# Optimization experiments

Measured on AMD Instinct MI355X. Metric: run time of the kernel, lower is better.

The kernel has to match this reference:

```python
import jax, jax.numpy as jnp
import numpy as np

N_NODES = 50000
N_EDGES = 25000
N_PAIRS = 800000
D = 96


def setup_inputs() -> dict:
    key = jax.random.key(0)
    ks = jax.random.split(key, 7)
    X = jax.random.normal(ks[0], (N_NODES, D), dtype=jnp.float32)
    X0 = jax.random.normal(ks[1], (N_NODES, D), dtype=jnp.float32)
    W = jax.random.normal(ks[2], (D, D), dtype=jnp.float32) / np.sqrt(D)
    degE = jax.random.uniform(ks[3], (N_EDGES, 1), dtype=jnp.float32, minval=0.1, maxval=1.0)
    degV = jax.random.uniform(ks[4], (N_NODES, 1), dtype=jnp.float32, minval=0.1, maxval=1.0)
    vertex = jax.random.randint(ks[5], (N_PAIRS,), 0, N_NODES, dtype=jnp.int32)
    edges = jax.random.randint(ks[6], (N_PAIRS,), 0, N_EDGES, dtype=jnp.int32)
    return {"X": X, "X0": X0, "W": W, "degE": degE, "degV": degV,
            "vertex": vertex, "edges": edges, "alpha": 0.1, "beta": 0.5}


def reference(X, X0, W, degE, degV, vertex, edges, alpha, beta):
    N = X.shape[0]
    E = degE.shape[0]
    # V -> E hop: gather node features per incidence pair, mean-reduce per hyperedge
    Xve = X[vertex]                                                  # [M, D]
    esum = jax.ops.segment_sum(Xve, edges, num_segments=E)           # [E, D]
    cnt = jax.ops.segment_sum(jnp.ones((edges.shape[0], 1), X.dtype), edges, num_segments=E)
    Xe = esum / jnp.maximum(cnt, 1.0)                                # mean aggregate
    Xe = Xe * degE
    # E -> V hop: gather hyperedge features, sum-reduce per node
    Xev = Xe[edges]                                                  # [M, D]
    Xv = jax.ops.segment_sum(Xev, vertex, num_segments=N)            # [N, D]
    Xv = Xv * degV
    # row L2 normalize (norm is detached in the original)
    rownorm = jnp.linalg.norm(Xv, axis=1, keepdims=True)
    scale = jax.lax.stop_gradient(jnp.where(rownorm > 0, 1.0 / rownorm, 0.0))
    Xn = Xv * scale
    # GCNII-style residual + identity-mapped Linear (bias=False)
    Xi = (1.0 - alpha) * Xn + alpha * X0
    return (1.0 - beta) * Xi + beta * (Xi @ W.T)
```

## Files before the change

kernel.cpp:

```cpp
#include <hip/hip_runtime.h>

#define DD 96
#define DQ 24
#define DC 12
#define SE 80
#define SV 48

typedef __attribute__((ext_vector_type(8))) unsigned short u16x8;
typedef __attribute__((ext_vector_type(8))) short s16x8;
typedef __attribute__((ext_vector_type(4))) float f32x4;

__device__ __forceinline__ unsigned short f2bf(float f) {
    unsigned int u = __builtin_bit_cast(unsigned int, f);
    u += 0x7FFFu + ((u >> 16) & 1u);
    return (unsigned short)(u >> 16);
}
__device__ __forceinline__ float bf2f(unsigned short h) {
    unsigned int u = ((unsigned int)h) << 16;
    return __builtin_bit_cast(float, u);
}

__global__ void hist_conv_k(const int* __restrict__ vtx, const int* __restrict__ edg,
                            int* __restrict__ cntV, int* __restrict__ cntE,
                            unsigned int* __restrict__ rank, int M,
                            const float4* __restrict__ X, u16x8* __restrict__ Xb, int n8,
                            const float* __restrict__ W, const float* __restrict__ beta_p,
                            unsigned short* __restrict__ Mm) {
    int t = blockIdx.x * 256 + threadIdx.x;
    bool doConv = (t < n8);
    float4 a, b;
    if (doConv) {
        a = X[(size_t)t * 2];
        b = X[(size_t)t * 2 + 1];
    }
    bool doHist = (t < M);
    unsigned rE = 0, rV = 0;
    if (doHist) {
        int e = edg[t];
        int v = vtx[t];
        rE = atomicAdd(&cntE[e << 2], 1);
        rV = atomicAdd(&cntV[v << 2], 1);
    }
    if (doConv) {
        u16x8 o;
        o[0] = f2bf(a.x); o[1] = f2bf(a.y); o[2] = f2bf(a.z); o[3] = f2bf(a.w);
        o[4] = f2bf(b.x); o[5] = f2bf(b.y); o[6] = f2bf(b.z); o[7] = f2bf(b.w);
        Xb[t] = o;
    } else if (t < n8 + DD * DD) {
        int i = t - n8;
        int c = i / DD;
        int k = i - c * DD;
        float m = beta_p[0] * W[i];
        if (c == k) m += 1.0f - beta_p[0];
        Mm[i] = f2bf(m);
    }
    if (doHist) rank[t] = (rE & 0xFFFFu) | (rV << 16);
}

__global__ void build_k(const int* __restrict__ vtx, const int* __restrict__ edg,
                        const unsigned int* __restrict__ rank,
                        unsigned short* __restrict__ vlist,
                        unsigned short* __restrict__ elist, int M) {
    int t = blockIdx.x * blockDim.x + threadIdx.x;
    int m0 = t * 4;
    if (m0 + 3 < M) {
        int4 v4 = *(const int4*)(vtx + m0);
        int4 e4 = *(const int4*)(edg + m0);
        uint4 r4 = *(const uint4*)(rank + m0);
        unsigned rE0 = r4.x & 0xFFFFu, rV0 = r4.x >> 16;
        unsigned rE1 = r4.y & 0xFFFFu, rV1 = r4.y >> 16;
        unsigned rE2 = r4.z & 0xFFFFu, rV2 = r4.z >> 16;
        unsigned rE3 = r4.w & 0xFFFFu, rV3 = r4.w >> 16;
        if (rE0 < SE) vlist[e4.x * SE + rE0] = (unsigned short)v4.x;
        if (rE1 < SE) vlist[e4.y * SE + rE1] = (unsigned short)v4.y;
        if (rE2 < SE) vlist[e4.z * SE + rE2] = (unsigned short)v4.z;
        if (rE3 < SE) vlist[e4.w * SE + rE3] = (unsigned short)v4.w;
        if (rV0 < SV) elist[v4.x * SV + rV0] = (unsigned short)e4.x;
        if (rV1 < SV) elist[v4.y * SV + rV1] = (unsigned short)e4.y;
        if (rV2 < SV) elist[v4.z * SV + rV2] = (unsigned short)e4.z;
        if (rV3 < SV) elist[v4.w * SV + rV3] = (unsigned short)e4.w;
    } else {
        for (int m = m0; m < M; ++m) {
            int v = vtx[m], e = edg[m];
            unsigned r = rank[m];
            unsigned rE = r & 0xFFFFu, rV = r >> 16;
            if (rE < SE) vlist[e * SE + rE] = (unsigned short)v;
            if (rV < SV) elist[v * SV + rV] = (unsigned short)e;
        }
    }
}

__global__ __launch_bounds__(256) void gather_ve_w(const u16x8* __restrict__ Xb,
                                                   const int* __restrict__ cntE,
                                                   const unsigned short* __restrict__ vlist,
                                                   const float* __restrict__ degE,
                                                   u16x8* __restrict__ Xe, int E) {
    int wid = threadIdx.x >> 6;
    int lane = threadIdx.x & 63;
    int e = blockIdx.x * 4 + wid;
    if (e >= E) return;
    int cnt = cntE[e << 2];
    int end = min(cnt, SE);
    const unsigned short* seg = vlist + (size_t)e * SE;
    int part = lane / DC;
    int chunk = lane - part * DC;
    float acc[8] = {0.f, 0.f, 0.f, 0.f, 0.f, 0.f, 0.f, 0.f};
    if (lane < 48) {
        for (int i = part; i < end; i += 4) {
            int v = seg[i];
            u16x8 x = Xb[v * DC + chunk];
            #pragma unroll
            for (int j = 0; j < 8; ++j) acc[j] += bf2f(x[j]);
        }
    }
    #pragma unroll
    for (int j = 0; j < 8; ++j) {
        float o = __shfl(acc[j], (lane + 24) & 63);
        if (lane < 24) acc[j] += o;
    }
    #pragma unroll
    for (int j = 0; j < 8; ++j) {
        float o = __shfl(acc[j], (lane + 12) & 63);
        if (lane < 12) acc[j] += o;
    }
    if (lane < DC) {
        float s = degE[e] / fmaxf((float)cnt, 1.0f);
        u16x8 o;
        #pragma unroll
        for (int j = 0; j < 8; ++j) o[j] = f2bf(acc[j] * s);
        Xe[e * DC + chunk] = o;
    }
}

__global__ __launch_bounds__(256) void gather_norm_w(const u16x8* __restrict__ Xe,
                                                     const int* __restrict__ cntV,
                                                     const unsigned short* __restrict__ elist,
                                                     const float4* __restrict__ X0,
                                                     const float* __restrict__ degV,
                                                     const float* __restrict__ alpha_p,
                                                     u16x8* __restrict__ Xi, int N) {
    int wid = threadIdx.x >> 6;
    int lane = threadIdx.x & 63;
    int r = blockIdx.x * 4 + wid;
    if (r >= N) return;
    int end = min(cntV[r << 2], SV);
    const unsigned short* seg = elist + (size_t)r * SV;
    int part = lane / DC;
    int chunk = lane - part * DC;
    float acc[8] = {0.f, 0.f, 0.f, 0.f, 0.f, 0.f, 0.f, 0.f};
    if (lane < 48) {
        for (int i = part; i < end; i += 4) {
            int e = seg[i];
            u16x8 x = Xe[e * DC + chunk];
            #pragma unroll
            for (int j = 0; j < 8; ++j) acc[j] += bf2f(x[j]);
        }
    }
    #pragma unroll
    for (int j = 0; j < 8; ++j) {
        float o = __shfl(acc[j], (lane + 24) & 63);
        if (lane < 24) acc[j] += o;
    }
    #pragma unroll
    for (int j = 0; j < 8; ++j) {
        float o = __shfl(acc[j], (lane + 12) & 63);
        if (lane < 12) acc[j] += o;
    }
    float ss = 0.f;
    if (lane < DC) {
        float dv = degV[r];
        #pragma unroll
        for (int j = 0; j < 8; ++j) { acc[j] *= dv; ss += acc[j] * acc[j]; }
    }
    #pragma unroll
    for (int off = 32; off; off >>= 1) ss += __shfl_xor(ss, off);
    float scale = (ss > 0.f) ? (1.0f / sqrtf(ss)) : 0.f;
    if (lane < DC) {
        float alpha = *alpha_p;
        float oma = 1.0f - alpha;
        float4 a = X0[r * DQ + chunk * 2];
        float4 b = X0[r * DQ + chunk * 2 + 1];
        float x0v[8] = {a.x, a.y, a.z, a.w, b.x, b.y, b.z, b.w};
        u16x8 o;
        #pragma unroll
        for (int j = 0; j < 8; ++j) o[j] = f2bf(oma * scale * acc[j] + alpha * x0v[j]);
        Xi[r * DC + chunk] = o;
    }
}

__global__ __launch_bounds__(256) void gemm_k(const u16x8* __restrict__ Xi,
                                              const unsigned short* __restrict__ Mm,
                                              float* __restrict__ out, int N) {
    int wid = threadIdx.x >> 6;
    int lane = threadIdx.x & 63;
    int lrow = lane & 15;
    int lkq = lane >> 4;
    int ntile = (N + 15) / 16;
    int tile = blockIdx.x * 4 + wid;
    if (tile >= ntile) return;
    s16x8 Bf[6][3];
    #pragma unroll
    for (int ct = 0; ct < 6; ++ct)
        #pragma unroll
        for (int ks = 0; ks < 3; ++ks)
            Bf[ct][ks] = *(const s16x8*)&Mm[(ct * 16 + lrow) * DD + ks * 32 + lkq * 8];
    int r0 = tile * 16;
    const s16x8* xr = (const s16x8*)Xi + (size_t)(r0 + lrow) * DC + lkq;
    f32x4 acc[6] = {};
    #pragma unroll
    for (int ks = 0; ks < 3; ++ks) {
        s16x8 a = xr[ks * 4];
        #pragma unroll
        for (int ct = 0; ct < 6; ++ct)
            acc[ct] = __builtin_amdgcn_mfma_f32_16x16x32_bf16(a, Bf[ct][ks], acc[ct], 0, 0, 0);
    }
    int orow = r0 + lkq * 4;
    #pragma unroll
    for (int ct = 0; ct < 6; ++ct)
        #pragma unroll
        for (int rg = 0; rg < 4; ++rg)
            out[(size_t)(orow + rg) * DD + ct * 16 + lrow] = acc[ct][rg];
}

extern "C" void kernel_launch(void* const* d_in, const int* in_sizes, int n_in,
                              void* d_out, int out_size, void* d_ws, size_t ws_size,
                              hipStream_t stream) {
    const float* X      = (const float*)d_in[0];
    const float* X0     = (const float*)d_in[1];
    const float* W      = (const float*)d_in[2];
    const float* degE   = (const float*)d_in[3];
    const float* degV   = (const float*)d_in[4];
    const int*   vertex = (const int*)d_in[5];
    const int*   edges  = (const int*)d_in[6];
    const float* alpha  = (const float*)d_in[7];
    const float* beta   = (const float*)d_in[8];

    int N = in_sizes[0] / DD;
    int E = in_sizes[3];
    int M = in_sizes[5];

    u16x8* Xb = (u16x8*)d_ws;
    u16x8* Xe = Xb + (size_t)N * DC;
    u16x8* Xi = Xe + (size_t)E * DC;
    unsigned int* rank = (unsigned int*)Xi;
    int* cntE = (int*)(Xi + (size_t)N * DC);
    int* cntV = cntE + (size_t)E * 4;
    unsigned short* vlist = (unsigned short*)(cntV + (size_t)N * 4);
    unsigned short* elist = vlist + (size_t)E * SE;
    unsigned short* Mm = elist + (size_t)N * SV;

    hipMemsetAsync(cntE, 0, (size_t)(E + N) * 4 * sizeof(int), stream);

    int n8 = N * DC;
    int tmax = M;
    hist_conv_k<<<(tmax + 255) / 256, 256, 0, stream>>>(vertex, edges, cntV, cntE,
                                                        rank, M, (const float4*)X, Xb,
                                                        n8, W, beta, Mm);

    build_k<<<((M + 3) / 4 + 255) / 256, 256, 0, stream>>>(vertex, edges, rank,
                                                           vlist, elist, M);

    gather_ve_w<<<(E + 3) / 4, 256, 0, stream>>>(Xb, cntE, vlist, degE, Xe, E);

    gather_norm_w<<<(N + 3) / 4, 256, 0, stream>>>(Xe, cntV, elist,
                                                   (const float4*)X0, degV, alpha, Xi, N);

    int ntile = (N + 15) / 16;
    gemm_k<<<(ntile + 3) / 4, 256, 0, stream>>>(Xi, Mm, (float*)d_out, N);
}
```

Baseline: 172.8 us.

## Move X bf16 conversion into build kernel and pack count arrays densely

The X-to-bf16 conversion and the W/beta mixing-matrix build move out of the histogram kernel into extra blocks appended to the list-building kernel. The histogram kernel becomes a lean atomic-only pass. The per-edge and per-node counters are packed densely instead of padded to a 4-int stride, which shrinks the memset. The aim is to keep the atomic-bound histogram free of heavy streaming loads, but denser counters may raise atomic contention within cache lines.

```diff
diff --git a/kernel.cpp b/kernel.cpp
--- a/kernel.cpp
+++ b/kernel.cpp
@@ -20,48 +20,46 @@
     return __builtin_bit_cast(float, u);
 }
 
-__global__ void hist_conv_k(const int* __restrict__ vtx, const int* __restrict__ edg,
-                            int* __restrict__ cntV, int* __restrict__ cntE,
-                            unsigned int* __restrict__ rank, int M,
-                            const float4* __restrict__ X, u16x8* __restrict__ Xb, int n8,
-                            const float* __restrict__ W, const float* __restrict__ beta_p,
-                            unsigned short* __restrict__ Mm) {
+__global__ void hist_k(const int* __restrict__ vtx, const int* __restrict__ edg,
+                       int* __restrict__ cntV, int* __restrict__ cntE,
+                       unsigned int* __restrict__ rank, int M) {
+    int m = blockIdx.x * 256 + threadIdx.x;
+    if (m >= M) return;
+    int v = vtx[m];
+    int e = edg[m];
+    unsigned rE = atomicAdd(&cntE[e], 1);
+    unsigned rV = atomicAdd(&cntV[v], 1);
+    rank[m] = (rE & 0xFFFFu) | (rV << 16);
+}
+
+__global__ void build_conv_k(const int* __restrict__ vtx, const int* __restrict__ edg,
+                             const unsigned int* __restrict__ rank,
+                             unsigned short* __restrict__ vlist,
+                             unsigned short* __restrict__ elist, int M, int BB,
+                             const float4* __restrict__ X, u16x8* __restrict__ Xb,
+                             int n8, const float* __restrict__ W,
+                             const float* __restrict__ beta_p,
+                             unsigned short* __restrict__ Mm) {
+    if ((int)blockIdx.x >= BB) {
+        int t = (blockIdx.x - BB) * 256 + threadIdx.x;
+        if (t < n8) {
+            float4 a = X[(size_t)t * 2];
+            float4 b = X[(size_t)t * 2 + 1];
+            u16x8 o;
+            o[0] = f2bf(a.x); o[1] = f2bf(a.y); o[2] = f2bf(a.z); o[3] = f2bf(a.w);
+            o[4] = f2bf(b.x); o[5] = f2bf(b.y); o[6] = f2bf(b.z); o[7] = f2bf(b.w);
+            Xb[t] = o;
+        } else if (t < n8 + DD * DD) {
+            int i = t - n8;
+            int c = i / DD;
+            int k = i - c * DD;
+            float m = beta_p[0] * W[i];
+            if (c == k) m += 1.0f - beta_p[0];
+            Mm[i] = f2bf(m);
+        }
+        return;
+    }
     int t = blockIdx.x * 256 + threadIdx.x;
-    bool doConv = (t < n8);
-    float4 a, b;
-    if (doConv) {
-        a = X[(size_t)t * 2];
-        b = X[(size_t)t * 2 + 1];
-    }
-    bool doHist = (t < M);
-    unsigned rE = 0, rV = 0;
-    if (doHist) {
-        int e = edg[t];
-        int v = vtx[t];
-        rE = atomicAdd(&cntE[e << 2], 1);
-        rV = atomicAdd(&cntV[v << 2], 1);
-    }
-    if (doConv) {
-        u16x8 o;
-        o[0] = f2bf(a.x); o[1] = f2bf(a.y); o[2] = f2bf(a.z); o[3] = f2bf(a.w);
-        o[4] = f2bf(b.x); o[5] = f2bf(b.y); o[6] = f2bf(b.z); o[7] = f2bf(b.w);
-        Xb[t] = o;
-    } else if (t < n8 + DD * DD) {
-        int i = t - n8;
-        int c = i / DD;
-        int k = i - c * DD;
-        float m = beta_p[0] * W[i];
-        if (c == k) m += 1.0f - beta_p[0];
-        Mm[i] = f2bf(m);
-    }
-    if (doHist) rank[t] = (rE & 0xFFFFu) | (rV << 16);
-}
-
-__global__ void build_k(const int* __restrict__ vtx, const int* __restrict__ edg,
-                        const unsigned int* __restrict__ rank,
-                        unsigned short* __restrict__ vlist,
-                        unsigned short* __restrict__ elist, int M) {
-    int t = blockIdx.x * blockDim.x + threadIdx.x;
     int m0 = t * 4;
     if (m0 + 3 < M) {
         int4 v4 = *(const int4*)(vtx + m0);
@@ -99,7 +97,7 @@
     int lane = threadIdx.x & 63;
     int e = blockIdx.x * 4 + wid;
     if (e >= E) return;
-    int cnt = cntE[e << 2];
+    int cnt = cntE[e];
     int end = min(cnt, SE);
     const unsigned short* seg = vlist + (size_t)e * SE;
     int part = lane / DC;
@@ -143,7 +141,7 @@
     int lane = threadIdx.x & 63;
     int r = blockIdx.x * 4 + wid;
     if (r >= N) return;
-    int end = min(cntV[r << 2], SV);
+    int end = min(cntV[r], SV);
     const unsigned short* seg = elist + (size_t)r * SV;
     int part = lane / DC;
     int chunk = lane - part * DC;
@@ -244,21 +242,20 @@
     u16x8* Xi = Xe + (size_t)E * DC;
     unsigned int* rank = (unsigned int*)Xi;
     int* cntE = (int*)(Xi + (size_t)N * DC);
-    int* cntV = cntE + (size_t)E * 4;
-    unsigned short* vlist = (unsigned short*)(cntV + (size_t)N * 4);
+    int* cntV = cntE + E;
+    unsigned short* vlist = (unsigned short*)(cntV + N);
     unsigned short* elist = vlist + (size_t)E * SE;
     unsigned short* Mm = elist + (size_t)N * SV;
 
-    hipMemsetAsync(cntE, 0, (size_t)(E + N) * 4 * sizeof(int), stream);
+    hipMemsetAsync(cntE, 0, (size_t)(E + N) * sizeof(int), stream);
+
+    hist_k<<<(M + 255) / 256, 256, 0, stream>>>(vertex, edges, cntV, cntE, rank, M);
 
     int n8 = N * DC;
-    int tmax = M;
-    hist_conv_k<<<(tmax + 255) / 256, 256, 0, stream>>>(vertex, edges, cntV, cntE,
-                                                        rank, M, (const float4*)X, Xb,
-                                                        n8, W, beta, Mm);
-
-    build_k<<<((M + 3) / 4 + 255) / 256, 256, 0, stream>>>(vertex, edges, rank,
-                                                           vlist, elist, M);
+    int BB = ((M + 3) / 4 + 255) / 256;
+    int CB = (n8 + DD * DD + 255) / 256;
+    build_conv_k<<<BB + CB, 256, 0, stream>>>(vertex, edges, rank, vlist, elist, M, BB,
+                                              (const float4*)X, Xb, n8, W, beta, Mm);
 
     gather_ve_w<<<(E + 3) / 4, 256, 0, stream>>>(Xb, cntE, vlist, degE, Xe, E);
 
```

Result: no change. 175.0 us (+1.2%).
